# Performance work log

Hardware: AMD Instinct MI355X
Metric: run time of the kernel (lower is better)

Reference implementation:

```python
import jax, jax.numpy as jnp
import numpy as np

N_NODES = 65536
N_EDGES = 1048576
F_IN = 64
F_OUT = 128
K = 3


def setup_inputs() -> dict:
    key = jax.random.key(0)
    k1, k2, k3, k4, k5 = jax.random.split(key, 5)
    X = jax.random.normal(k1, (N_NODES, F_IN), dtype=jnp.float32)
    edge_row = jax.random.randint(k2, (N_EDGES,), 0, N_NODES, dtype=jnp.int32)
    edge_col = jax.random.randint(k3, (N_EDGES,), 0, N_NODES, dtype=jnp.int32)
    # rescaled-Laplacian values; scale down so the K-step recurrence stays bounded
    edge_val = jax.random.normal(k4, (N_EDGES,), dtype=jnp.float32) * 0.05
    W = jax.random.normal(k5, (F_IN * K, F_OUT), dtype=jnp.float32) * (1.0 / np.sqrt(F_IN * K))
    b = jnp.zeros((F_OUT,), dtype=jnp.float32)
    return {"X": X, "edge_row": edge_row, "edge_col": edge_col,
            "edge_val": edge_val, "W": W, "b": b}


def reference(X, edge_row, edge_col, edge_val, W, b):
    # Sparse L @ Y via gather + segment-sum over COO edges (irregular access).
    N = X.shape[0]

    def spmm(Y):
        # [E, F] gathered messages, scattered back to rows
        msgs = edge_val[:, None] * Y[edge_col]
        return jax.ops.segment_sum(msgs, edge_row, num_segments=N)

    # Chebyshev recurrence: T0 = X, T1 = L X, T_k = 2 L T_{k-1} - T_{k-2}
    T_prev2 = X
    T_prev1 = spmm(X)
    terms = [T_prev2, T_prev1]
    for _ in range(2, K):
        T_next = 2.0 * spmm(T_prev1) - T_prev2
        terms.append(T_next)
        T_prev2, T_prev1 = T_prev1, T_next

    H = jnp.concatenate(terms[:K], axis=-1)  # [N, K*Fin]
    # Linear; dropout is identity at eval / p=0
    return H @ W + b
```

## Files before the change

### kernel.cpp

```cpp
#include <hip/hip_runtime.h>

#define N_NODES 65536
#define N_EDGES 1048576
#define F_IN 64
#define F_OUT 128
#define KDIM (F_IN * 3)
#define NB 1024

typedef float f32x4 __attribute__((ext_vector_type(4)));
typedef short bf16x8 __attribute__((ext_vector_type(8)));

static __device__ __forceinline__ unsigned short f2bf(float f)
{
    unsigned u = __float_as_uint(f);
    u += 0x7FFFu + ((u >> 16) & 1u);
    return (unsigned short)(u >> 16);
}
static __device__ __forceinline__ float bf2f(unsigned short h)
{
    return __uint_as_float((unsigned)h << 16);
}


__global__ __launch_bounds__(256) void wpack(const float* __restrict__ W,
                                             unsigned short* __restrict__ Wp)
{
    int p = blockIdx.x * 256 + threadIdx.x;
    int j   = p & 7;
    int gx  = (p >> 3) & 3;
    int c15 = (p >> 5) & 15;
    int n   = (p >> 9) & 7;
    int kk  = p >> 12;
    int g   = gx ^ (c15 & 3);
    int k   = kk * 32 + g * 8 + j;
    int c   = n * 16 + c15;
    Wp[p] = f2bf(W[k * F_OUT + c]);
}

__global__ __launch_bounds__(256) void xconvert(const float* __restrict__ X,
                                                unsigned short* __restrict__ Xb)
{
    unsigned i = (blockIdx.x * 256u + threadIdx.x) * 4u;
    float4 x = *(const float4*)(X + i);
    ushort4 o;
    o.x = f2bf(x.x); o.y = f2bf(x.y); o.z = f2bf(x.z); o.w = f2bf(x.w);
    *(ushort4*)(Xb + i) = o;
}


__global__ __launch_bounds__(256) void zero_bcur(int* __restrict__ bcur)
{
    ((int4*)bcur)[threadIdx.x] = make_int4(0, 0, 0, 0);
}

__global__ __launch_bounds__(256) void bucket_hist(const int* __restrict__ erow,
                                                   int* __restrict__ bcur)
{
    __shared__ int h[NB];
    int t = threadIdx.x;
    for (int i = t; i < NB; i += 256) h[i] = 0;
    __syncthreads();
    int base = blockIdx.x * 8192;
    for (int j = 0; j < 8; ++j) {
        int4 r = *(const int4*)(erow + base + j * 1024 + t * 4);
        atomicAdd(&h[r.x >> 6], 1);
        atomicAdd(&h[r.y >> 6], 1);
        atomicAdd(&h[r.z >> 6], 1);
        atomicAdd(&h[r.w >> 6], 1);
    }
    __syncthreads();
    for (int i = t; i < NB; i += 256)
        if (h[i]) atomicAdd(&bcur[i], h[i]);
}

__global__ __launch_bounds__(256) void scan_buckets(int* __restrict__ bcur,
                                                    int* __restrict__ boff)
{
    __shared__ int s[256];
    int t = threadIdx.x;
    int4 c = ((const int4*)bcur)[t];
    int tsum = c.x + c.y + c.z + c.w;
    s[t] = tsum;
    __syncthreads();
    for (int d = 1; d < 256; d <<= 1) {
        int v = (t >= d) ? s[t - d] : 0;
        __syncthreads();
        s[t] += v;
        __syncthreads();
    }
    int run = s[t] - tsum;
    int4 o;
    o.x = run;
    o.y = o.x + c.x;
    o.z = o.y + c.y;
    o.w = o.z + c.z;
    ((int4*)boff)[t] = o;
    ((int4*)bcur)[t] = o;
    if (t == 255) boff[NB] = N_EDGES;
}

__global__ __launch_bounds__(256) void bucketize(
    const int* __restrict__ erow, const int* __restrict__ ecol,
    const float* __restrict__ eval, int* __restrict__ bcur,
    int2* __restrict__ bent)
{
    __shared__ int h[NB];
    __shared__ int gbase[NB];
    int t = threadIdx.x;
    for (int i = t; i < NB; i += 256) h[i] = 0;
    __syncthreads();
    int base = blockIdx.x * 8192;
    for (int j = 0; j < 8; ++j) {
        int4 r = *(const int4*)(erow + base + j * 1024 + t * 4);
        atomicAdd(&h[r.x >> 6], 1);
        atomicAdd(&h[r.y >> 6], 1);
        atomicAdd(&h[r.z >> 6], 1);
        atomicAdd(&h[r.w >> 6], 1);
    }
    __syncthreads();
    for (int i = t; i < NB; i += 256) {
        int cnt = h[i];
        gbase[i] = cnt ? atomicAdd(&bcur[i], cnt) : 0;
        h[i] = 0;
    }
    __syncthreads();
    for (int j = 0; j < 8; ++j) {
        int4   r = *(const int4*)(erow + base + j * 1024 + t * 4);
        int4   c = *(const int4*)(ecol + base + j * 1024 + t * 4);
        float4 v = *(const float4*)(eval + base + j * 1024 + t * 4);
        {
            int b = r.x >> 6; int p = atomicAdd(&h[b], 1);
            bent[gbase[b] + p] = make_int2((int)(((unsigned)r.x << 16) | (unsigned)c.x), __float_as_int(v.x));
        }
        {
            int b = r.y >> 6; int p = atomicAdd(&h[b], 1);
            bent[gbase[b] + p] = make_int2((int)(((unsigned)r.y << 16) | (unsigned)c.y), __float_as_int(v.y));
        }
        {
            int b = r.z >> 6; int p = atomicAdd(&h[b], 1);
            bent[gbase[b] + p] = make_int2((int)(((unsigned)r.z << 16) | (unsigned)c.z), __float_as_int(v.z));
        }
        {
            int b = r.w >> 6; int p = atomicAdd(&h[b], 1);
            bent[gbase[b] + p] = make_int2((int)(((unsigned)r.w << 16) | (unsigned)c.w), __float_as_int(v.w));
        }
    }
}

__global__ __launch_bounds__(256) void build_csr(
    const int* __restrict__ boff, const int2* __restrict__ bent,
    int* __restrict__ off, int2* __restrict__ csr)
{
    __shared__ int rh[64];
    __shared__ int rbase[64];
    int b = blockIdx.x;
    int t = threadIdx.x;
    int s = boff[b];
    int e = boff[b + 1];
    int n = e - s;
    if (t < 64) rh[t] = 0;
    __syncthreads();
    for (int i = t; i < n; i += 256) {
        unsigned rc = (unsigned)bent[s + i].x;
        atomicAdd(&rh[(rc >> 16) & 63], 1);
    }
    __syncthreads();
    if (t == 0) {
        int run = s;
        for (int k = 0; k < 64; ++k) { rbase[k] = run; run += rh[k]; }
    }
    __syncthreads();
    if (t < 64) {
        off[b * 64 + t] = rbase[t];
        rh[t] = 0;
    }
    if (b == NB - 1 && t == 0) off[N_NODES] = N_EDGES;
    __syncthreads();
    for (int i = t; i < n; i += 256) {
        int2 en = bent[s + i];
        unsigned rc = (unsigned)en.x;
        int rl = (rc >> 16) & 63;
        int p = atomicAdd(&rh[rl], 1);
        csr[rbase[rl] + p] = make_int2((int)(rc & 0xFFFFu), en.y);
    }
}

template <int MODE>
__global__ __launch_bounds__(256) void spmm_b(
    const int* __restrict__ off, const int2* __restrict__ csr,
    const unsigned short* __restrict__ Yb, const float* __restrict__ X,
    unsigned short* __restrict__ outb)
{
    int r    = blockIdx.x * 4 + (threadIdx.x >> 6);
    int lane = threadIdx.x & 63;
    int s = off[r];
    int e = off[r + 1];
    float a0 = 0.f, a1 = 0.f, a2 = 0.f, a3 = 0.f;
    int i = s;
    for (; i + 4 <= e; i += 4) {
        int2 e0 = csr[i];
        int2 e1 = csr[i + 1];
        int2 e2 = csr[i + 2];
        int2 e3 = csr[i + 3];
        float y0 = bf2f(Yb[(size_t)e0.x * F_IN + lane]);
        float y1 = bf2f(Yb[(size_t)e1.x * F_IN + lane]);
        float y2 = bf2f(Yb[(size_t)e2.x * F_IN + lane]);
        float y3 = bf2f(Yb[(size_t)e3.x * F_IN + lane]);
        a0 = fmaf(__int_as_float(e0.y), y0, a0);
        a1 = fmaf(__int_as_float(e1.y), y1, a1);
        a2 = fmaf(__int_as_float(e2.y), y2, a2);
        a3 = fmaf(__int_as_float(e3.y), y3, a3);
    }
    for (; i < e; ++i) {
        int2 ed = csr[i];
        a0 = fmaf(__int_as_float(ed.y), bf2f(Yb[(size_t)ed.x * F_IN + lane]), a0);
    }
    float acc = (a0 + a1) + (a2 + a3);
    size_t o = (size_t)r * F_IN + lane;
    if (MODE == 2) acc = 2.f * acc - X[o];
    outb[o] = f2bf(acc);
}

__global__ __launch_bounds__(512) void gemm_mfma(
    const unsigned short* __restrict__ Xb, const unsigned short* __restrict__ T1b,
    const unsigned short* __restrict__ T2b, const unsigned short* __restrict__ Wp,
    const float* __restrict__ bias, float* __restrict__ out)
{
    __shared__ __align__(16) unsigned short Wl[24576];
    int t = threadIdx.x;
    for (int i = t; i < 3072; i += 512)
        ((float4*)Wl)[i] = ((const float4*)Wp)[i];
    __syncthreads();

    int w   = t >> 6;
    int l   = t & 63;
    int c15 = l & 15;
    int g   = l >> 4;
    int brow = blockIdx.x * 128 + w * 16;
    int arow = brow + c15;

    const unsigned short* srcs[3] = {Xb, T1b, T2b};
    bf16x8 a[6];
    #pragma unroll
    for (int kk = 0; kk < 6; ++kk) {
        const unsigned short* src = srcs[kk >> 1];
        a[kk] = *(const bf16x8*)(src + (size_t)arow * F_IN + (kk & 1) * 32 + g * 8);
    }

    f32x4 acc[8];
    #pragma unroll
    for (int n = 0; n < 8; ++n) acc[n] = (f32x4){0.f, 0.f, 0.f, 0.f};

    int gx = g ^ (c15 & 3);
    #pragma unroll
    for (int kk = 0; kk < 6; ++kk) {
        #pragma unroll
        for (int n = 0; n < 8; ++n) {
            int idx = (((kk * 8 + n) * 16 + c15) * 4 + gx) * 8;
            bf16x8 b = *(const bf16x8*)&Wl[idx];
            acc[n] = __builtin_amdgcn_mfma_f32_16x16x32_bf16(a[kk], b, acc[n], 0, 0, 0);
        }
    }

    #pragma unroll
    for (int n = 0; n < 8; ++n) {
        float bv = bias[n * 16 + c15];
        #pragma unroll
        for (int r = 0; r < 4; ++r) {
            int orow = brow + g * 4 + r;
            out[(size_t)orow * F_OUT + n * 16 + c15] = acc[n][r] + bv;
        }
    }
}

extern "C" void kernel_launch(void* const* d_in, const int* in_sizes, int n_in,
                              void* d_out, int out_size, void* d_ws, size_t ws_size,
                              hipStream_t stream)
{
    const float* X    = (const float*)d_in[0];
    const int*   erow = (const int*)  d_in[1];
    const int*   ecol = (const int*)  d_in[2];
    const float* eval = (const float*)d_in[3];
    const float* W    = (const float*)d_in[4];
    const float* bias = (const float*)d_in[5];
    float* out = (float*)d_out;

    unsigned short* Xb  = (unsigned short*)d_ws;
    unsigned short* T1b = Xb  + (size_t)N_NODES * F_IN;
    unsigned short* T2b = T1b + (size_t)N_NODES * F_IN;
    unsigned short* Wp  = T2b + (size_t)N_NODES * F_IN;

    int*  off  = (int*)d_out;
    int2* csr  = (int2*)(off + 65600);
    int*  boff = (int*)(csr + N_EDGES);
    int*  bcur = boff + 1088;
    int2* bent = (int2*)(bcur + 1024);

    wpack<<<96, 256, 0, stream>>>(W, Wp);
    xconvert<<<N_NODES * F_IN / 4 / 256, 256, 0, stream>>>(X, Xb);

    zero_bcur<<<1, 256, 0, stream>>>(bcur);
    bucket_hist<<<128, 256, 0, stream>>>(erow, bcur);
    scan_buckets<<<1, 256, 0, stream>>>(bcur, boff);
    bucketize<<<128, 256, 0, stream>>>(erow, ecol, eval, bcur, bent);
    build_csr<<<NB, 256, 0, stream>>>(boff, bent, off, csr);

    spmm_b<1><<<N_NODES / 4, 256, 0, stream>>>(off, csr, Xb, X, T1b);
    spmm_b<2><<<N_NODES / 4, 256, 0, stream>>>(off, csr, T1b, X, T2b);

    gemm_mfma<<<N_NODES / 128, 512, 0, stream>>>(Xb, T1b, T2b, Wp, bias, out);
}
```

Measured before the change: 218.2 us.

## Fuse CSR build with first SpMM and unroll gather loops by eight

The CSR build kernel now also computes T1 = L·X. It keeps each 64-row bucket's entries in shared memory and has each wave reduce 16 rows, which removes a separate launch and the global re-read of the CSR for the first SpMM. The second SpMM and the fused kernel both unroll the gather loop to eight independent accumulators, putting more loads in flight. The shared buffer has a fixed capacity of 1536 entries per bucket (about 1024 expected), so a bucket larger than that would overflow. The fused kernel also runs only 1024 blocks, which may lower parallelism for the gathers.

```diff
diff --git a/kernel.cpp b/kernel.cpp
--- a/kernel.cpp
+++ b/kernel.cpp
@@ -4,8 +4,8 @@
 #define N_EDGES 1048576
 #define F_IN 64
 #define F_OUT 128
-#define KDIM (F_IN * 3)
 #define NB 1024
+#define ENT_CAP 1536
 
 typedef float f32x4 __attribute__((ext_vector_type(4)));
 typedef short bf16x8 __attribute__((ext_vector_type(8)));
@@ -147,12 +147,14 @@
     }
 }
 
-__global__ __launch_bounds__(256) void build_csr(
+__global__ __launch_bounds__(256) void build_spmm1(
     const int* __restrict__ boff, const int2* __restrict__ bent,
-    int* __restrict__ off, int2* __restrict__ csr)
+    int* __restrict__ off, int2* __restrict__ csr,
+    const unsigned short* __restrict__ Xb, unsigned short* __restrict__ T1b)
 {
     __shared__ int rh[64];
     __shared__ int rbase[64];
+    __shared__ int2 ent[ENT_CAP];
     int b = blockIdx.x;
     int t = threadIdx.x;
     int s = boff[b];
@@ -160,18 +162,16 @@
     int n = e - s;
     if (t < 64) rh[t] = 0;
     __syncthreads();
-    for (int i = t; i < n; i += 256) {
-        unsigned rc = (unsigned)bent[s + i].x;
-        atomicAdd(&rh[(rc >> 16) & 63], 1);
-    }
+    for (int i = t; i < n; i += 256)
+        atomicAdd(&rh[((unsigned)bent[s + i].x >> 16) & 63], 1);
     __syncthreads();
     if (t == 0) {
-        int run = s;
+        int run = 0;
         for (int k = 0; k < 64; ++k) { rbase[k] = run; run += rh[k]; }
     }
     __syncthreads();
     if (t < 64) {
-        off[b * 64 + t] = rbase[t];
+        off[b * 64 + t] = s + rbase[t];
         rh[t] = 0;
     }
     if (b == NB - 1 && t == 0) off[N_NODES] = N_EDGES;
@@ -180,13 +180,54 @@
         int2 en = bent[s + i];
         unsigned rc = (unsigned)en.x;
         int rl = (rc >> 16) & 63;
-        int p = atomicAdd(&rh[rl], 1);
-        csr[rbase[rl] + p] = make_int2((int)(rc & 0xFFFFu), en.y);
-    }
-}
-
-template <int MODE>
-__global__ __launch_bounds__(256) void spmm_b(
+        int p = rbase[rl] + atomicAdd(&rh[rl], 1);
+        int2 cv = make_int2((int)(rc & 0xFFFFu), en.y);
+        ent[p] = cv;
+        csr[s + p] = cv;
+    }
+    __syncthreads();
+    int wv   = t >> 6;
+    int lane = t & 63;
+    for (int rr = 0; rr < 16; ++rr) {
+        int rl = wv * 16 + rr;
+        int ls = rbase[rl];
+        int le = ls + rh[rl];
+        float a0 = 0.f, a1 = 0.f, a2 = 0.f, a3 = 0.f;
+        float a4 = 0.f, a5 = 0.f, a6 = 0.f, a7 = 0.f;
+        int i = ls;
+        for (; i + 8 <= le; i += 8) {
+            int2 e0 = ent[i];     int2 e1 = ent[i + 1];
+            int2 e2 = ent[i + 2]; int2 e3 = ent[i + 3];
+            int2 e4 = ent[i + 4]; int2 e5 = ent[i + 5];
+            int2 e6 = ent[i + 6]; int2 e7 = ent[i + 7];
+            float y0 = bf2f(Xb[(size_t)e0.x * F_IN + lane]);
+            float y1 = bf2f(Xb[(size_t)e1.x * F_IN + lane]);
+            float y2 = bf2f(Xb[(size_t)e2.x * F_IN + lane]);
+            float y3 = bf2f(Xb[(size_t)e3.x * F_IN + lane]);
+            float y4 = bf2f(Xb[(size_t)e4.x * F_IN + lane]);
+            float y5 = bf2f(Xb[(size_t)e5.x * F_IN + lane]);
+            float y6 = bf2f(Xb[(size_t)e6.x * F_IN + lane]);
+            float y7 = bf2f(Xb[(size_t)e7.x * F_IN + lane]);
+            a0 = fmaf(__int_as_float(e0.y), y0, a0);
+            a1 = fmaf(__int_as_float(e1.y), y1, a1);
+            a2 = fmaf(__int_as_float(e2.y), y2, a2);
+            a3 = fmaf(__int_as_float(e3.y), y3, a3);
+            a4 = fmaf(__int_as_float(e4.y), y4, a4);
+            a5 = fmaf(__int_as_float(e5.y), y5, a5);
+            a6 = fmaf(__int_as_float(e6.y), y6, a6);
+            a7 = fmaf(__int_as_float(e7.y), y7, a7);
+        }
+        for (; i < le; ++i) {
+            int2 ed = ent[i];
+            a0 = fmaf(__int_as_float(ed.y), bf2f(Xb[(size_t)ed.x * F_IN + lane]), a0);
+        }
+        float acc = ((a0 + a1) + (a2 + a3)) + ((a4 + a5) + (a6 + a7));
+        int r = b * 64 + rl;
+        T1b[(size_t)r * F_IN + lane] = f2bf(acc);
+    }
+}
+
+__global__ __launch_bounds__(256) void spmm2(
     const int* __restrict__ off, const int2* __restrict__ csr,
     const unsigned short* __restrict__ Yb, const float* __restrict__ X,
     unsigned short* __restrict__ outb)
@@ -196,29 +237,45 @@
     int s = off[r];
     int e = off[r + 1];
     float a0 = 0.f, a1 = 0.f, a2 = 0.f, a3 = 0.f;
+    float a4 = 0.f, a5 = 0.f, a6 = 0.f, a7 = 0.f;
     int i = s;
-    for (; i + 4 <= e; i += 4) {
-        int2 e0 = csr[i];
-        int2 e1 = csr[i + 1];
-        int2 e2 = csr[i + 2];
-        int2 e3 = csr[i + 3];
+    for (; i + 8 <= e; i += 8) {
+        int2 e0 = csr[i];     int2 e1 = csr[i + 1];
+        int2 e2 = csr[i + 2]; int2 e3 = csr[i + 3];
+        int2 e4 = csr[i + 4]; int2 e5 = csr[i + 5];
+        int2 e6 = csr[i + 6]; int2 e7 = csr[i + 7];
         float y0 = bf2f(Yb[(size_t)e0.x * F_IN + lane]);
         float y1 = bf2f(Yb[(size_t)e1.x * F_IN + lane]);
         float y2 = bf2f(Yb[(size_t)e2.x * F_IN + lane]);
         float y3 = bf2f(Yb[(size_t)e3.x * F_IN + lane]);
+        float y4 = bf2f(Yb[(size_t)e4.x * F_IN + lane]);
+        float y5 = bf2f(Yb[(size_t)e5.x * F_IN + lane]);
+        float y6 = bf2f(Yb[(size_t)e6.x * F_IN + lane]);
+        float y7 = bf2f(Yb[(size_t)e7.x * F_IN + lane]);
         a0 = fmaf(__int_as_float(e0.y), y0, a0);
         a1 = fmaf(__int_as_float(e1.y), y1, a1);
         a2 = fmaf(__int_as_float(e2.y), y2, a2);
         a3 = fmaf(__int_as_float(e3.y), y3, a3);
+        a4 = fmaf(__int_as_float(e4.y), y4, a4);
+        a5 = fmaf(__int_as_float(e5.y), y5, a5);
+        a6 = fmaf(__int_as_float(e6.y), y6, a6);
+        a7 = fmaf(__int_as_float(e7.y), y7, a7);
+    }
+    for (; i + 4 <= e; i += 4) {
+        int2 e0 = csr[i];     int2 e1 = csr[i + 1];
+        int2 e2 = csr[i + 2]; int2 e3 = csr[i + 3];
+        a0 = fmaf(__int_as_float(e0.y), bf2f(Yb[(size_t)e0.x * F_IN + lane]), a0);
+        a1 = fmaf(__int_as_float(e1.y), bf2f(Yb[(size_t)e1.x * F_IN + lane]), a1);
+        a2 = fmaf(__int_as_float(e2.y), bf2f(Yb[(size_t)e2.x * F_IN + lane]), a2);
+        a3 = fmaf(__int_as_float(e3.y), bf2f(Yb[(size_t)e3.x * F_IN + lane]), a3);
     }
     for (; i < e; ++i) {
         int2 ed = csr[i];
         a0 = fmaf(__int_as_float(ed.y), bf2f(Yb[(size_t)ed.x * F_IN + lane]), a0);
     }
-    float acc = (a0 + a1) + (a2 + a3);
+    float acc = ((a0 + a1) + (a2 + a3)) + ((a4 + a5) + (a6 + a7));
     size_t o = (size_t)r * F_IN + lane;
-    if (MODE == 2) acc = 2.f * acc - X[o];
-    outb[o] = f2bf(acc);
+    outb[o] = f2bf(2.f * acc - X[o]);
 }
 
 __global__ __launch_bounds__(512) void gemm_mfma(
@@ -303,10 +360,9 @@
     bucket_hist<<<128, 256, 0, stream>>>(erow, bcur);
     scan_buckets<<<1, 256, 0, stream>>>(bcur, boff);
     bucketize<<<128, 256, 0, stream>>>(erow, ecol, eval, bcur, bent);
-    build_csr<<<NB, 256, 0, stream>>>(boff, bent, off, csr);
-
-    spmm_b<1><<<N_NODES / 4, 256, 0, stream>>>(off, csr, Xb, X, T1b);
-    spmm_b<2><<<N_NODES / 4, 256, 0, stream>>>(off, csr, T1b, X, T2b);
+
+    build_spmm1<<<NB, 256, 0, stream>>>(boff, bent, off, csr, Xb, T1b);
+    spmm2<<<N_NODES / 4, 256, 0, stream>>>(off, csr, T1b, X, T2b);
 
     gemm_mfma<<<N_NODES / 128, 512, 0, stream>>>(Xb, T1b, T2b, Wp, bias, out);
 }
```

Measured after the change: 214.9 us. About the same (-1.5%).
